# Optimization experiments

Hardware: AMD Instinct MI355X
Metric: run time of the kernel (lower is better)

## Reference

```python
import jax, jax.numpy as jnp
import numpy as np

B, T, H, W = 4, 8, 256, 256


def _shift(u, axis, d):
    """Value at index i comes from i+d along `axis`; zero (Dirichlet) boundary."""
    if d == 0:
        return u
    pad = [(0, 0)] * u.ndim
    sl = [slice(None)] * u.ndim
    if d > 0:
        sl[axis] = slice(d, None)
        pad[axis] = (0, d)
    else:
        sl[axis] = slice(None, d)
        pad[axis] = (-d, 0)
    return jnp.pad(u[tuple(sl)], pad)


def custom_sigmoid(x, mn, mx):
    # matches NLL.custom_sigmoid: (sigmoid(x) + min/(max-min)) * (max-min)
    return (jax.nn.sigmoid(x) + mn / (mx - mn)) * (mx - mn)


def setup_inputs() -> dict:
    key = jax.random.key(0)
    k1, k2 = jax.random.split(key)
    x = jax.random.normal(k1, (B, T, H, W), dtype=jnp.float32)
    conv_w = jax.random.normal(k2, (8 * T, T, 3, 3), dtype=jnp.float32) * 0.05
    return {"x": x, "conv_w": conv_w}


def reference(x, conv_w):
    Bn, Tn, Hn, Wn = x.shape
    dt = dx = dy = 1.0  # st_lag = [1,1,1]

    # Encoder: Conv2d(n_t -> 8*n_t, 3x3, padding=1, bias=False)
    theta = jax.lax.conv_general_dilated(
        x, conv_w, window_strides=(1, 1), padding="SAME",
        dimension_numbers=("NCHW", "OIHW", "NCHW"))

    # reshape_params: split 8*n_t channels into SPDE fields, bounded to valid ranges
    kappa = custom_sigmoid(theta[:, :Tn], 0.01, 1.0)          # damping
    m1 = theta[:, Tn:2 * Tn]                                   # advection x
    m2 = theta[:, 2 * Tn:3 * Tn]                               # advection y
    Hxx = custom_sigmoid(theta[:, 3 * Tn:4 * Tn], 0.01, 1.0)  # diffusion tensor
    Hxy = 0.1 * jnp.tanh(theta[:, 4 * Tn:5 * Tn])
    Hyx = 0.1 * jnp.tanh(theta[:, 5 * Tn:6 * Tn])
    Hyy = custom_sigmoid(theta[:, 6 * Tn:7 * Tn], 0.01, 1.0)
    tau = custom_sigmoid(theta[:, 7 * Tn:8 * Tn], 0.1, 10.0)   # noise scale

    # finite-difference stencils (zero Dirichlet boundary), vectorized over (B,T)
    def Dx(u):
        return (_shift(u, -1, 1) - _shift(u, -1, -1)) / (2 * dx)

    def Dy(u):
        return (_shift(u, -2, 1) - _shift(u, -2, -1)) / (2 * dy)

    def Dxx(u):
        return (_shift(u, -1, 1) + _shift(u, -1, -1) - 2 * u) / (dx * dx)

    def Dyy(u):
        return (_shift(u, -2, 1) + _shift(u, -2, -1) - 2 * u) / (dy * dy)

    def A(u):
        # advection-diffusion operator: kappa^2 u + m.grad u - div(H grad u)
        return ((kappa * kappa) * u + m1 * Dx(u) + m2 * Dy(u)
                - (Hxx * Dxx(u) + Hyy * Dyy(u) + (Hxy + Hyx) * Dx(Dy(u))))

    # pow=1 -> alpha=2 -> B = A^2 ; M_k = I + dt * B_k
    Mx = x + dt * A(A(x))                      # [B,T,H,W], M_k x_k for all k

    # Q = L^T D L with L block-bidiagonal (L[k,k]=M_k, L[k,k-1]=-I),
    # D_k = diag(dt / tau_k^2)  (inv_tau = sqrt(dt)/tau in create_Q)
    x_prev = jnp.concatenate([jnp.zeros_like(x[:, :1]), x[:, :-1]], axis=1)
    r = Mx - x_prev                            # r_k = M_k x_k - x_{k-1}
    D = dt / (tau * tau)

    xQx = jnp.sum(D * r * r)                   # quadratic form x^T Q x
    logdetD = jnp.sum(jnp.log(D))              # diagonal log-det contribution
    return 0.5 * (xQx - logdetD)
```

## Files before the change

kernel.cpp:

```cpp
#include <hip/hip_runtime.h>

#define F_ELEMS 2097152
#define IMG 65536

typedef _Float16 half8  __attribute__((ext_vector_type(8)));
typedef _Float16 half2v __attribute__((ext_vector_type(2)));
typedef _Float16 half4v __attribute__((ext_vector_type(4)));
typedef float    floatx4 __attribute__((ext_vector_type(4)));

__device__ __forceinline__ float sigm(float x){ return 1.0f/(1.0f + __expf(-x)); }
__device__ __forceinline__ float tanh_fast(float x){
    float t = __expf(2.0f*x);
    return 1.0f - 2.0f/(t + 1.0f);
}

__global__ __launch_bounds__(256) void conv_mfma(
    const float* __restrict__ x, const float* __restrict__ w,
    _Float16* __restrict__ fld, float* __restrict__ out)
{
    __shared__ _Float16 xt[4*258*8];
    __shared__ _Float16 Wl[12*64*8];

    const int tid = threadIdx.x;
    const int i0  = blockIdx.x << 1;
    const int b   = blockIdx.y;

    if (tid == 0 && blockIdx.x == 0 && blockIdx.y == 0) out[0] = 0.0f;

    for (int e = tid; e < 258*4*4; e += 256){
        int cc = e % 258;
        int rr = (e/258) & 3;
        int cp = e / (258*4);
        int gi = i0 - 1 + rr, gj = cc - 1;
        float v0 = 0.0f, v1 = 0.0f;
        if (gi >= 0 && gi < 256 && gj >= 0 && gj < 256){
            int base = ((b*8 + 2*cp) << 16) + (gi << 8) + gj;
            v0 = x[base];
            v1 = x[base + IMG];
        }
        half2v h; h[0] = (_Float16)v0; h[1] = (_Float16)v1;
        *(half2v*)&xt[(rr*258 + cc)*8 + 2*cp] = h;
    }
    for (int e = tid; e < 12*64*8; e += 256){
        int c  = e & 7;
        int oc = (e >> 3) & 63;
        int t  = e >> 9;
        float v = (t < 9) ? w[(oc*8 + c)*9 + t] : 0.0f;
        Wl[e] = (_Float16)v;
    }
    __syncthreads();

    const int lane = tid & 63;
    const int quad = lane >> 4;
    const int l16  = lane & 15;
    const int wv   = tid >> 6;

    half8 afr[4][3];
    int boff[3];
    #pragma unroll
    for (int s = 0; s < 3; ++s){
        int t  = s*4 + quad;
        afr[0][s] = *(const half8*)&Wl[(t*64 +  0 + l16)*8];
        afr[1][s] = *(const half8*)&Wl[(t*64 + 16 + l16)*8];
        afr[2][s] = *(const half8*)&Wl[(t*64 + 32 + l16)*8];
        afr[3][s] = *(const half8*)&Wl[(t*64 + 48 + l16)*8];
        int tc = (t < 9) ? t : 8;
        int dh = tc / 3, dw = tc - dh*3;
        boff[s] = (dh*258 + dw)*8;
    }

    const bool lo  = (l16 < 8);
    const int  tlo = l16 << 16, thi = (l16 - 8) << 16;
    const int  off0 = lo ? (0*F_ELEMS + tlo) : (1*F_ELEMS + thi);
    const int  off1 = lo ? (2*F_ELEMS + tlo) : (3*F_ELEMS + thi);
    const int  off2 = 4*F_ELEMS + tlo;
    const int  off3 = lo ? (5*F_ELEMS + tlo) : (6*F_ELEMS + thi);

    #pragma unroll 2
    for (int it = 0; it < 8; ++it){
        const int g   = it*4 + wv;
        const int r   = g >> 4;
        const int jb  = ((g & 15) << 4) + l16;
        const int xoff = (r*258 + jb)*8;

        floatx4 acc0 = {0,0,0,0}, acc1 = {0,0,0,0}, acc2 = {0,0,0,0}, acc3 = {0,0,0,0};
        #pragma unroll
        for (int s = 0; s < 3; ++s){
            half8 bf = *(const half8*)&xt[xoff + boff[s]];
            acc0 = __builtin_amdgcn_mfma_f32_16x16x32_f16(bf, afr[0][s], acc0, 0, 0, 0);
            acc1 = __builtin_amdgcn_mfma_f32_16x16x32_f16(bf, afr[1][s], acc1, 0, 0, 0);
            acc2 = __builtin_amdgcn_mfma_f32_16x16x32_f16(bf, afr[2][s], acc2, 0, 0, 0);
            acc3 = __builtin_amdgcn_mfma_f32_16x16x32_f16(bf, afr[3][s], acc3, 0, 0, 0);
        }

        const int jb0  = (g & 15) << 4;
        const int pixb = (b << 19) + ((i0 + r) << 8) + jb0 + (quad << 2);

        half4v h0, h1, h2, h3;
        #pragma unroll
        for (int rg = 0; rg < 4; ++rg){
            float v0 = acc0[rg];
            float s0 = 0.99f*sigm(v0) + 0.01f;
            h0[rg] = (_Float16)(lo ? s0*s0 : v0);
            float v1 = acc1[rg];
            h1[rg] = (_Float16)(lo ? v1 : 0.99f*sigm(v1) + 0.01f);
            float th  = 0.1f*tanh_fast(acc2[rg]);
            float oth = __shfl_xor(th, 8, 64);
            h2[rg] = (_Float16)(th + oth);
            float sg = sigm(acc3[rg]);
            h3[rg] = (_Float16)(lo ? 0.99f*sg + 0.01f : 9.9f*sg + 0.1f);
        }
        *(half4v*)&fld[off0 + pixb] = h0;
        *(half4v*)&fld[off1 + pixb] = h1;
        if (lo) *(half4v*)&fld[off2 + pixb] = h2;
        *(half4v*)&fld[off3 + pixb] = h3;
    }
}

__device__ __forceinline__ void ldf4(const _Float16* __restrict__ p, float o[4]){
    half4v h = *(const half4v*)p;
    o[0] = (float)h[0]; o[1] = (float)h[1]; o[2] = (float)h[2]; o[3] = (float)h[3];
}

__device__ __forceinline__ void row6(const float* __restrict__ u, int rb, int j0, float v[6]){
    const float4 c4 = *(const float4*)&u[rb + j0];
    v[1] = c4.x; v[2] = c4.y; v[3] = c4.z; v[4] = c4.w;
    v[0] = (j0 > 0)   ? u[rb + j0 - 1] : 0.0f;
    v[5] = (j0 < 252) ? u[rb + j0 + 4] : 0.0f;
}

__device__ __forceinline__ void stencil4(const float k2[4], const float m1[4],
    const float m2[4], const float hx[4], const float hs[4], const float hy[4],
    const float vc[6], const float vn[6], const float vs[6], float rp[4])
{
    #pragma unroll
    for (int p = 0; p < 4; ++p){
        float hxx = hx[p], hyy = hy[p];
        rp[p] = (k2[p] + 2.0f*(hxx + hyy))*vc[p+1]
              + (0.5f*m1[p] - hxx)*vc[p+2]
              - (0.5f*m1[p] + hxx)*vc[p]
              + (0.5f*m2[p] - hyy)*vn[p+1]
              - (0.5f*m2[p] + hyy)*vs[p+1]
              - 0.25f*hs[p]*(vn[p+2] - vs[p+2] - vn[p] + vs[p]);
    }
}

#define YSW 268
__global__ __launch_bounds__(256) void fused_A(
    const float* __restrict__ x, const _Float16* __restrict__ fld,
    float* __restrict__ out)
{
    __shared__ float ys[18*YSW];
    __shared__ float redA[4], redB[4];

    const int tid = threadIdx.x;
    const int cg  = tid & 63;
    const int rw  = tid >> 6;
    const int jc  = cg << 2;
    const int bt  = blockIdx.y;
    const int t   = bt & 7;
    const int i0  = blockIdx.x << 4;

    if (tid < 18){ ys[tid*YSW + 3] = 0.0f; ys[tid*YSW + 260] = 0.0f; }

    for (int p = 0; p < 5; ++p){
        int yr = p*4 + rw;
        if (yr < 18){
            int iy = i0 - 1 + yr;
            float y[4] = {0,0,0,0};
            if (iy >= 0 && iy < 256){
                int pix = (bt << 16) + (iy << 8) + jc;
                int rb  = pix - jc;
                float vc[6], vn[6], vs[6];
                row6(x, rb, jc, vc);
                if (iy < 255) row6(x, rb + 256, jc, vn);
                else { vn[0]=vn[1]=vn[2]=vn[3]=vn[4]=vn[5]=0.0f; }
                if (iy > 0) row6(x, rb - 256, jc, vs);
                else { vs[0]=vs[1]=vs[2]=vs[3]=vs[4]=vs[5]=0.0f; }
                float k2[4], m1[4], m2[4], hx[4], hs[4], hy[4];
                ldf4(&fld[0*F_ELEMS + pix], k2);
                ldf4(&fld[1*F_ELEMS + pix], m1);
                ldf4(&fld[2*F_ELEMS + pix], m2);
                ldf4(&fld[3*F_ELEMS + pix], hx);
                ldf4(&fld[4*F_ELEMS + pix], hs);
                ldf4(&fld[5*F_ELEMS + pix], hy);
                stencil4(k2, m1, m2, hx, hs, hy, vc, vn, vs, y);
            }
            float4 y4 = make_float4(y[0], y[1], y[2], y[3]);
            *(float4*)&ys[yr*YSW + 4 + jc] = y4;
        }
    }
    __syncthreads();

    float local = 0.0f;
    float lprod = 1.0f;
    #pragma unroll
    for (int p = 0; p < 4; ++p){
        int zr = p*4 + rw;
        int iz = i0 + zr;
        int pix = (bt << 16) + (iz << 8) + jc;
        int base = (zr + 1)*YSW + 4 + jc;

        float vc[6], vn[6], vs[6];
        {
            float4 c4 = *(const float4*)&ys[base];
            vc[1]=c4.x; vc[2]=c4.y; vc[3]=c4.z; vc[4]=c4.w;
            vc[0]=ys[base-1]; vc[5]=ys[base+4];
            float4 n4 = *(const float4*)&ys[base+YSW];
            vn[1]=n4.x; vn[2]=n4.y; vn[3]=n4.z; vn[4]=n4.w;
            vn[0]=ys[base+YSW-1]; vn[5]=ys[base+YSW+4];
            float4 s4 = *(const float4*)&ys[base-YSW];
            vs[1]=s4.x; vs[2]=s4.y; vs[3]=s4.z; vs[4]=s4.w;
            vs[0]=ys[base-YSW-1]; vs[5]=ys[base-YSW+4];
        }
        float k2[4], m1[4], m2[4], hx[4], hs[4], hy[4], tv[4], z[4];
        ldf4(&fld[0*F_ELEMS + pix], k2);
        ldf4(&fld[1*F_ELEMS + pix], m1);
        ldf4(&fld[2*F_ELEMS + pix], m2);
        ldf4(&fld[3*F_ELEMS + pix], hx);
        ldf4(&fld[4*F_ELEMS + pix], hs);
        ldf4(&fld[5*F_ELEMS + pix], hy);
        ldf4(&fld[6*F_ELEMS + pix], tv);
        stencil4(k2, m1, m2, hx, hs, hy, vc, vn, vs, z);

        float4 xc = *(const float4*)&x[pix];
        float4 xp = make_float4(0,0,0,0);
        if (t > 0) xp = *(const float4*)&x[pix - IMG];
        const float* xcp = (const float*)&xc;
        const float* xpp = (const float*)&xp;
        #pragma unroll
        for (int q = 0; q < 4; ++q){
            float r = xcp[q] + z[q] - xpp[q];
            float dq = 1.0f/(tv[q]*tv[q]);
            local += dq*r*r;
        }
        lprod *= tv[0]*tv[1];
        lprod *= tv[2]*tv[3];
    }

    float a = local;
    float b = __logf(lprod);
    #pragma unroll
    for (int off = 32; off > 0; off >>= 1){
        a += __shfl_down(a, off);
        b += __shfl_down(b, off);
    }
    if (cg == 0){ redA[rw] = a; redB[rw] = b; }
    __syncthreads();
    if (tid == 0){
        float ra = redA[0] + redA[1] + redA[2] + redA[3];
        float rb = redB[0] + redB[1] + redB[2] + redB[3];
        atomicAdd(out, 0.5f*ra + rb);
    }
}

extern "C" void kernel_launch(void* const* d_in, const int* in_sizes, int n_in,
                              void* d_out, int out_size, void* d_ws, size_t ws_size,
                              hipStream_t stream)
{
    const float* x = (const float*)d_in[0];
    const float* w = (const float*)d_in[1];
    float* out = (float*)d_out;
    _Float16* fld = (_Float16*)d_ws;

    conv_mfma<<<dim3(128, 4), 256, 0, stream>>>(x, w, fld, out);
    fused_A<<<dim3(16, 32), 256, 0, stream>>>(x, fld, out);
}
```

Baseline: 99.38 us.

## Merge conv and stencil kernels into one cooperative launch with grid sync

Wraps the convolution and fused stencil bodies as device functions and runs both in a single cooperative kernel of 512 blocks, separated by a threadfence and a grid-wide sync. This is meant to remove the second kernel launch and the gap between the two kernels. The price is a grid barrier and combined shared-memory use per block, which can lower occupancy. If the cooperative launch fails, the code falls back to the original two kernels.

```diff
diff --git a/kernel.cpp b/kernel.cpp
--- a/kernel.cpp
+++ b/kernel.cpp
@@ -1,4 +1,7 @@
 #include <hip/hip_runtime.h>
+#include <hip/hip_cooperative_groups.h>
+
+namespace cg = cooperative_groups;
 
 #define F_ELEMS 2097152
 #define IMG 65536
@@ -14,18 +17,17 @@
     return 1.0f - 2.0f/(t + 1.0f);
 }
 
-__global__ __launch_bounds__(256) void conv_mfma(
+
+__device__ __forceinline__ void conv_body(
     const float* __restrict__ x, const float* __restrict__ w,
-    _Float16* __restrict__ fld, float* __restrict__ out)
-{
-    __shared__ _Float16 xt[4*258*8];
-    __shared__ _Float16 Wl[12*64*8];
-
+    _Float16* __restrict__ fld, float* __restrict__ out,
+    int strip, int b, int zero_flag,
+    _Float16* xt , _Float16* Wl )
+{
     const int tid = threadIdx.x;
-    const int i0  = blockIdx.x << 1;
-    const int b   = blockIdx.y;
-
-    if (tid == 0 && blockIdx.x == 0 && blockIdx.y == 0) out[0] = 0.0f;
+    const int i0  = strip << 1;
+
+    if (zero_flag && tid == 0) out[0] = 0.0f;
 
     for (int e = tid; e < 258*4*4; e += 256){
         int cc = e % 258;
@@ -146,20 +148,17 @@
 }
 
 #define YSW 268
-__global__ __launch_bounds__(256) void fused_A(
+__device__ __forceinline__ void fused_body(
     const float* __restrict__ x, const _Float16* __restrict__ fld,
-    float* __restrict__ out)
-{
-    __shared__ float ys[18*YSW];
-    __shared__ float redA[4], redB[4];
-
+    float* __restrict__ out, int istrip, int bt,
+    float* ys , float* redA , float* redB )
+{
     const int tid = threadIdx.x;
     const int cg  = tid & 63;
     const int rw  = tid >> 6;
     const int jc  = cg << 2;
-    const int bt  = blockIdx.y;
     const int t   = bt & 7;
-    const int i0  = blockIdx.x << 4;
+    const int i0  = istrip << 4;
 
     if (tid < 18){ ys[tid*YSW + 3] = 0.0f; ys[tid*YSW + 260] = 0.0f; }
 
@@ -254,6 +253,44 @@
     }
 }
 
+__global__ __launch_bounds__(256) void mega(
+    const float* __restrict__ x, const float* __restrict__ w,
+    _Float16* __restrict__ fld, float* __restrict__ out)
+{
+    __shared__ _Float16 xt[4*258*8];
+    __shared__ _Float16 Wl[12*64*8];
+    __shared__ float ys[18*YSW];
+    __shared__ float redA[4], redB[4];
+
+    const int bid = blockIdx.x;
+
+    conv_body(x, w, fld, out, bid & 127, bid >> 7, bid == 0, xt, Wl);
+
+    __threadfence();
+    cg::this_grid().sync();
+
+    fused_body(x, fld, out, bid & 15, bid >> 4, ys, redA, redB);
+}
+
+__global__ __launch_bounds__(256) void conv_mfma(
+    const float* __restrict__ x, const float* __restrict__ w,
+    _Float16* __restrict__ fld, float* __restrict__ out)
+{
+    __shared__ _Float16 xt[4*258*8];
+    __shared__ _Float16 Wl[12*64*8];
+    conv_body(x, w, fld, out, blockIdx.x, blockIdx.y,
+              (blockIdx.x == 0 && blockIdx.y == 0), xt, Wl);
+}
+
+__global__ __launch_bounds__(256) void fused_A(
+    const float* __restrict__ x, const _Float16* __restrict__ fld,
+    float* __restrict__ out)
+{
+    __shared__ float ys[18*YSW];
+    __shared__ float redA[4], redB[4];
+    fused_body(x, fld, out, blockIdx.x, blockIdx.y, ys, redA, redB);
+}
+
 extern "C" void kernel_launch(void* const* d_in, const int* in_sizes, int n_in,
                               void* d_out, int out_size, void* d_ws, size_t ws_size,
                               hipStream_t stream)
@@ -263,6 +300,11 @@
     float* out = (float*)d_out;
     _Float16* fld = (_Float16*)d_ws;
 
-    conv_mfma<<<dim3(128, 4), 256, 0, stream>>>(x, w, fld, out);
-    fused_A<<<dim3(16, 32), 256, 0, stream>>>(x, fld, out);
-}
+    void* args[] = { (void*)&x, (void*)&w, (void*)&fld, (void*)&out };
+    hipError_t err = hipLaunchCooperativeKernel(
+        (const void*)mega, dim3(512), dim3(256), args, 0, stream);
+    if (err != hipSuccess){
+        conv_mfma<<<dim3(128, 4), 256, 0, stream>>>(x, w, fld, out);
+        fused_A<<<dim3(16, 32), 256, 0, stream>>>(x, fld, out);
+    }
+}
```

Result: slower. 239.0 us (+140.4%).
